# Optimization experiments

Measured on AMD Instinct MI355X. Metric: run time of the kernel, lower is better.

## Reference

```python
import jax, jax.numpy as jnp
import numpy as np

B, T, D, H = 4, 2048, 1024, 16
DK, DV, CHUNK = D // H, 2 * D // H, 64  # head_k_dim=64, head_v_dim=128 (expand_v=2.0)
EPS = 1e-5


def setup_inputs() -> dict:
    key = jax.random.key(0)
    ks = jax.random.split(key, 6)
    s = 0.02
    return {
        "x": jax.random.normal(ks[0], (B, T, D), jnp.float32),
        "Wq": jax.random.normal(ks[1], (D, H * DK), jnp.float32) * s,
        "Wk": jax.random.normal(ks[2], (D, H * DK), jnp.float32) * s,
        "Wv": jax.random.normal(ks[3], (D, H * DV), jnp.float32) * s,
        "Wg": jax.random.normal(ks[4], (D, H * DV), jnp.float32) * s,
        "Wo": jax.random.normal(ks[5], (H * DV, D), jnp.float32) * s,
        "g_norm_w": jnp.ones((DV,), jnp.float32),
    }


def _rope(q):
    # q: [B, T, H, DK]; non-interleaved (rotate-half) rotary, base 10000
    half = DK // 2
    inv_freq = 1.0 / (10000.0 ** (jnp.arange(half, dtype=jnp.float32) / half))
    freqs = jnp.arange(T, dtype=jnp.float32)[:, None] * inv_freq  # [T, half]
    cos = jnp.cos(freqs)[None, :, None, :]
    sin = jnp.sin(freqs)[None, :, None, :]
    q1, q2 = q[..., :half], q[..., half:]
    return jnp.concatenate([q1 * cos - q2 * sin, q2 * cos + q1 * sin], axis=-1)


def reference(x, Wq, Wk, Wv, Wg, Wo, g_norm_w):
    q = _rope((x @ Wq).reshape(B, T, H, DK)) * (DK ** -0.5)
    k = _rope((x @ Wk).reshape(B, T, H, DK))
    v = (x @ Wv).reshape(B, T, H, DV)

    N = T // CHUNK
    def tochunks(t):  # [B,T,H,Dh] -> [N,B,H,C,Dh]
        return t.reshape(B, N, CHUNK, H, t.shape[-1]).transpose(1, 0, 3, 2, 4)
    qc, kc, vc = tochunks(q), tochunks(k), tochunks(v)

    # per-head RetNet decay: gamma_h = 1 - 2^{-5-h}
    gamma = 1.0 - jnp.exp2(-5.0 - jnp.arange(H, dtype=jnp.float32))  # [H]
    i = jnp.arange(CHUNK, dtype=jnp.float32)
    # intra-chunk decay mask D[h,i,j] = gamma^{i-j} for j<=i else 0
    Dmask = jnp.where(i[:, None] >= i[None, :],
                      gamma[:, None, None] ** (i[:, None] - i[None, :]), 0.0)  # [H,C,C]
    cross = gamma[:, None] ** (i + 1.0)          # [H,C] query decay vs prev state
    kdec = gamma[:, None] ** (CHUNK - 1.0 - i)   # [H,C] key decay into new state
    chunk_dec = gamma ** CHUNK                   # [H]

    def step(S, qkv):
        q_, k_, v_ = qkv  # [B,H,C,DK], [B,H,C,DK], [B,H,C,DV]
        attn = jnp.einsum('bhid,bhjd->bhij', q_, k_) * Dmask
        o = jnp.einsum('bhij,bhjv->bhiv', attn, v_)
        o = o + jnp.einsum('bhid,bhdv->bhiv', q_ * cross[None, :, :, None], S)
        S = S * chunk_dec[None, :, None, None] + \
            jnp.einsum('bhjd,bhjv->bhdv', k_ * kdec[None, :, :, None], v_)
        return S, o

    S0 = jnp.zeros((B, H, DK, DV), x.dtype)
    _, o = jax.lax.scan(step, S0, (qc, kc, vc))  # [N,B,H,C,DV]
    o = o.transpose(1, 0, 3, 2, 4).reshape(B, T, H, DV)

    # fused RMSNorm + swish gate (FusedRMSNormSwishGate)
    g = (x @ Wg).reshape(B, T, H, DV)
    o = o * jax.lax.rsqrt(jnp.mean(o * o, axis=-1, keepdims=True) + EPS) * g_norm_w
    o = o * (g * jax.nn.sigmoid(g))
    return o.reshape(B, T, H * DV) @ Wo
```

## Files before the change

### kernel.cpp

```cpp
#include <hip/hip_runtime.h>
#include <hip/hip_bf16.h>
#include <math.h>

typedef unsigned short u16;
typedef unsigned int u32;
typedef __attribute__((ext_vector_type(8))) short bf16x8;
typedef __attribute__((ext_vector_type(4))) float f32x4;


__device__ __forceinline__ u16 f2bf(float f) {
  union { float f; unsigned u; } a; a.f = f;
  unsigned u = a.u;
  unsigned r = (u + 0x7fffu + ((u >> 16) & 1u)) >> 16;
  return (u16)r;
}
__device__ __forceinline__ float bf2f(u16 s) {
  union { unsigned u; float f; } a; a.u = ((unsigned)s) << 16; return a.f;
}

__global__ void k_sentinel(float* out) {
  if (threadIdx.x == 0 && blockIdx.x == 0) out[0] = 1.0e6f;
}

__device__ __forceinline__ void split8r(const float* t, bf16x8& hi, bf16x8& lo) {
#pragma unroll
  for (int m = 0; m < 8; ++m) {
    union { float f; u32 u; } c; c.f = t[m];
    union { u32 u; float f; } hf; hf.u = c.u & 0xffff0000u;
    union { float f; u32 u; } lw; lw.f = t[m] - hf.f;
    hi[m] = (short)(u16)(c.u >> 16);
    lo[m] = (short)(u16)(lw.u >> 16);
  }
}
__device__ __forceinline__ void split8p(const float* __restrict__ p, bf16x8& hi, bf16x8& lo) {
  f32x4 a = *(const f32x4*)p;
  f32x4 b = *(const f32x4*)(p + 4);
  float t[8];
  t[0]=a[0]; t[1]=a[1]; t[2]=a[2]; t[3]=a[3]; t[4]=b[0]; t[5]=b[1]; t[6]=b[2]; t[7]=b[3];
  split8r(t, hi, lo);
}

__device__ __forceinline__ void bar_lds() {
  asm volatile("s_waitcnt lgkmcnt(0)" ::: "memory");
  __builtin_amdgcn_sched_barrier(0);
  __builtin_amdgcn_s_barrier();
}

__device__ __forceinline__ void gload16(const u16* g, u16* l) {
  __builtin_amdgcn_global_load_lds(
      (const __attribute__((address_space(1))) unsigned int*)g,
      (__attribute__((address_space(3))) unsigned int*)l, 16, 0, 0);
}

__global__ __launch_bounds__(256) void k_cvt_x(const float* __restrict__ src, u16* __restrict__ dst) {
  int i = blockIdx.x * 256 + threadIdx.x;
  float4 v = ((const float4*)src)[i];
  ushort4 o;
  o.x = f2bf(v.x); o.y = f2bf(v.y); o.z = f2bf(v.z); o.w = f2bf(v.w);
  ((ushort4*)dst)[i] = o;
}

__global__ __launch_bounds__(256) void k_transpose(const float* __restrict__ src, u16* __restrict__ dst,
                                                   int K, int N) {
  __shared__ float tile[32][33];
  int n0 = blockIdx.x * 32, k0 = blockIdx.y * 32;
  int tx = threadIdx.x & 31, ty = threadIdx.x >> 5;
  for (int r = 0; r < 32; r += 8)
    tile[ty + r][tx] = src[(size_t)(k0 + ty + r) * N + n0 + tx];
  __syncthreads();
  for (int r = 0; r < 32; r += 8)
    dst[(size_t)(n0 + ty + r) * K + k0 + tx] = f2bf(tile[tx][ty + r]);
}

template <bool BF16OUT>
__global__ __launch_bounds__(256, 2) void k_gemm(const u16* __restrict__ A, const u16* __restrict__ Bt,
                                                 void* __restrict__ Cv, int N, int K) {
  __shared__ __attribute__((aligned(16))) u16 As[128 * 32];
  __shared__ __attribute__((aligned(16))) u16 Bs[128 * 32];
  int nbx = gridDim.x;
  int id = blockIdx.y * nbx + blockIdx.x;
  int cpx = (nbx * gridDim.y) >> 3;
  int sw = (id & 7) * cpx + (id >> 3);
  int bx = sw % nbx, by = sw / nbx;
  int i0 = by * 128, n0 = bx * 128;
  int tid = threadIdx.x;
  int lane = tid & 63, w = tid >> 6;
  int wr = (w >> 1) * 64, wc = (w & 1) * 64;
  int srow = lane >> 2, scol = (lane & 3) * 8;
  f32x4 acc[4][4];
#pragma unroll
  for (int m = 0; m < 4; ++m)
#pragma unroll
    for (int n = 0; n < 4; ++n) acc[m][n] = (f32x4){0.f, 0.f, 0.f, 0.f};
  int fr = lane & 15, kb = (lane >> 4) * 8;
  for (int k0 = 0; k0 < K; k0 += 32) {
    __syncthreads();
#pragma unroll
    for (int q = 0; q < 2; ++q) {
      int s = w * 2 + q;
      gload16(&A[(size_t)(i0 + s * 16 + srow) * K + k0 + scol], &As[s * 512]);
      gload16(&Bt[(size_t)(n0 + s * 16 + srow) * K + k0 + scol], &Bs[s * 512]);
    }
    asm volatile("s_waitcnt vmcnt(0)" ::: "memory");
    __syncthreads();
    bf16x8 af[4], bfr[4];
#pragma unroll
    for (int m = 0; m < 4; ++m) af[m] = *(const bf16x8*)&As[(wr + m * 16 + fr) * 32 + kb];
#pragma unroll
    for (int n = 0; n < 4; ++n) bfr[n] = *(const bf16x8*)&Bs[(wc + n * 16 + fr) * 32 + kb];
#pragma unroll
    for (int m = 0; m < 4; ++m)
#pragma unroll
      for (int n = 0; n < 4; ++n)
        acc[m][n] = __builtin_amdgcn_mfma_f32_16x16x32_bf16(af[m], bfr[n], acc[m][n], 0, 0, 0);
  }
  int rb = (lane >> 4) * 4, cb = lane & 15;
#pragma unroll
  for (int m = 0; m < 4; ++m)
#pragma unroll
    for (int n = 0; n < 4; ++n) {
      int gr = i0 + wr + m * 16 + rb;
      int gc = n0 + wc + n * 16 + cb;
#pragma unroll
      for (int r = 0; r < 4; ++r) {
        float v = acc[m][n][r];
        if (BF16OUT) ((u16*)Cv)[(size_t)(gr + r) * N + gc] = f2bf(v);
        else         ((float*)Cv)[(size_t)(gr + r) * N + gc] = v;
      }
    }
}

__global__ __launch_bounds__(256) void k_rope(float* __restrict__ qk) {
  int idx = blockIdx.x * 256 + threadIdx.x;
  int i = idx & 31;
  int row = idx >> 5;
  int t = row & 2047;
  float invf = powf(10000.f, -(float)i * (1.f / 32.f));
  float fr = (float)t * invf;
  float s = sinf(fr), c = cosf(fr);
  float* p = qk + (size_t)row * 2048;
#pragma unroll
  for (int h = 0; h < 16; ++h) {
    int c1 = h * 64 + i, c2 = c1 + 32;
    float q1 = p[c1], q2 = p[c2];
    p[c1] = (q1 * c - q2 * s) * 0.125f;
    p[c2] = (q2 * c + q1 * s) * 0.125f;
    float k1 = p[1024 + c1], k2 = p[1024 + c2];
    p[1024 + c1] = k1 * c - k2 * s;
    p[1024 + c2] = k2 * c + k1 * s;
  }
}

__global__ __launch_bounds__(512) void k_retention(const float* __restrict__ qk, const u16* __restrict__ vg,
                                                   const float* __restrict__ gnw, u16* __restrict__ og) {
  int bh = blockIdx.x & 63, rq = blockIdx.x >> 6;
  int h = bh & 15, b = bh >> 4;
  int gi0 = rq * 16;

  __shared__ __attribute__((aligned(16))) float qs[16][68];
  __shared__ __attribute__((aligned(16))) float ks[64][68];
  __shared__ __attribute__((aligned(16))) u16 vst[128][88];
  __shared__ __attribute__((aligned(16))) u16 kta_h[8][520];
  __shared__ __attribute__((aligned(16))) u16 kta_l[8][520];
  __shared__ __attribute__((aligned(16))) u16 pa_h[8][136];
  __shared__ __attribute__((aligned(16))) u16 pa_l[8][136];
  __shared__ __attribute__((aligned(16))) u16 sst_h[8][1040];
  __shared__ __attribute__((aligned(16))) u16 sst_l[8][1040];
  __shared__ float dpow[72];
  __shared__ float ssred[8][16];

  int tid = threadIdx.x;
  int w = tid >> 6, l = tid & 63;
  int fr = l & 15, fq = l >> 4;
  float gamma = 1.f - exp2f(-5.f - (float)h);
  if (tid <= 64) dpow[tid] = powf(gamma, (float)tid);
  for (int c = tid; c < 4160; c += 512) { ((u32*)sst_h)[c] = 0; ((u32*)sst_l)[c] = 0; }
  __syncthreads();
  float cdec = dpow[64];

  int e0 = w * 16;
  float gww = gnw[e0 + fr];
  int khmax = (rq < 2) ? 1 : 2;

  int qi = tid >> 4, qd4 = (tid & 15) * 4;
  int sj = tid >> 3, sdg = (tid & 7) * 8;
  int vjp = tid & 31, ve8 = (tid >> 5) * 8;

  f32x4 Sacc[4][2];
#pragma unroll
  for (int dt = 0; dt < 4; ++dt)
#pragma unroll
    for (int nt = 0; nt < 2; ++nt) Sacc[dt][nt] = (f32x4){0.f, 0.f, 0.f, 0.f};

  f32x4 pq = (f32x4){0.f, 0.f, 0.f, 0.f};
  f32x4 pk0, pk1;
  bf16x8 pva, pvb;
  {
    int rowbase = b * 2048;
    if (tid < 256) pq = *(const f32x4*)&qk[(size_t)(rowbase + gi0 + qi) * 2048 + h * 64 + qd4];
    const float* kr = &qk[(size_t)(rowbase + sj) * 2048 + 1024 + h * 64 + sdg];
    pk0 = *(const f32x4*)kr;
    pk1 = *(const f32x4*)(kr + 4);
    const u16* vr = &vg[(size_t)(rowbase + 2 * vjp) * 4096 + h * 128 + ve8];
    pva = *(const bf16x8*)vr;
    pvb = *(const bf16x8*)(vr + 4096);
  }

  for (int n = 0; n < 32; ++n) {
    int rowbase = b * 2048 + n * 64;
    if (tid < 256) *(f32x4*)&qs[qi][qd4] = pq;
    {
      *(f32x4*)&ks[sj][sdg] = pk0;
      *(f32x4*)&ks[sj][sdg + 4] = pk1;
      float kdv = dpow[63 - sj];
      float kd[8];
#pragma unroll
      for (int m = 0; m < 4; ++m) { kd[m] = pk0[m] * kdv; kd[m + 4] = pk1[m] * kdv; }
      bf16x8 kh8, kl8;
      split8r(kd, kh8, kl8);
      int J = sj >> 3, s = sj & 7, dh = tid & 7;
#pragma unroll
      for (int m = 0; m < 8; ++m) {
        int blk = (dh * 8) | (m ^ dh);
        kta_h[J][blk * 8 + s] = (u16)kh8[m];
        kta_l[J][blk * 8 + s] = (u16)kl8[m];
      }
#pragma unroll
      for (int m = 0; m < 8; ++m)
        *(u32*)&vst[ve8 + m][2 * vjp] = (u32)(u16)pva[m] | ((u32)(u16)pvb[m] << 16);
    }
    __syncthreads();
    if (n < 31) {
      int rb2 = rowbase + 64;
      if (tid < 256) pq = *(const f32x4*)&qk[(size_t)(rb2 + gi0 + qi) * 2048 + h * 64 + qd4];
      const float* kr = &qk[(size_t)(rb2 + sj) * 2048 + 1024 + h * 64 + sdg];
      pk0 = *(const f32x4*)kr;
      pk1 = *(const f32x4*)(kr + 4);
      const u16* vr = &vg[(size_t)(rb2 + 2 * vjp) * 4096 + h * 128 + ve8];
      pva = *(const bf16x8*)vr;
      pvb = *(const bf16x8*)(vr + 4096);
    }
    if (w < 4) {
      int ct = w;
      f32x4 at = (f32x4){0.f, 0.f, 0.f, 0.f};
      if (16 * ct <= gi0 + 15) {
#pragma unroll
        for (int kh = 0; kh < 2; ++kh) {
          bf16x8 qh, ql, kbh, kbl;
          split8p(&qs[fr][kh * 32 + fq * 8], qh, ql);
          split8p(&ks[16 * ct + fr][kh * 32 + fq * 8], kbh, kbl);
          at = __builtin_amdgcn_mfma_f32_16x16x32_bf16(qh, kbh, at, 0, 0, 0);
          at = __builtin_amdgcn_mfma_f32_16x16x32_bf16(qh, kbl, at, 0, 0, 0);
          at = __builtin_amdgcn_mfma_f32_16x16x32_bf16(ql, kbh, at, 0, 0, 0);
        }
      }
      int j = 16 * ct + fr;
      int J = j >> 3, jc = j & 7;
#pragma unroll
      for (int r = 0; r < 4; ++r) {
        int i = fq * 4 + r, s = gi0 + i - j;
        float val = (s >= 0) ? at[r] * dpow[s] : 0.f;
        union { float f; u32 u; } c; c.f = val;
        union { u32 u; float f; } hf; hf.u = c.u & 0xffff0000u;
        union { float f; u32 u; } lw; lw.f = val - hf.f;
        pa_h[J][i * 8 + jc] = (u16)(c.u >> 16);
        pa_l[J][i * 8 + jc] = (u16)(lw.u >> 16);
      }
    } else if (n < 31) {
      int eb = (w - 4) * 32;
#pragma unroll
      for (int dt = 0; dt < 4; ++dt)
#pragma unroll
        for (int nt = 0; nt < 2; ++nt)
#pragma unroll
          for (int r = 0; r < 4; ++r) Sacc[dt][nt][r] *= cdec;
      bf16x8 bv[2][2];
#pragma unroll
      for (int kh2 = 0; kh2 < 2; ++kh2)
#pragma unroll
        for (int nt = 0; nt < 2; ++nt)
          bv[kh2][nt] = *(const bf16x8*)&vst[eb + nt * 16 + fr][kh2 * 32 + fq * 8];
#pragma unroll
      for (int kh2 = 0; kh2 < 2; ++kh2) {
#pragma unroll
        for (int dt = 0; dt < 4; ++dt) {
          int d = dt * 16 + fr;
          int blk = d ^ ((dt * 2 + (fr >> 3)) & 7);
          bf16x8 ah = *(const bf16x8*)&kta_h[kh2 * 4 + fq][blk * 8];
          bf16x8 al = *(const bf16x8*)&kta_l[kh2 * 4 + fq][blk * 8];
#pragma unroll
          for (int nt = 0; nt < 2; ++nt) {
            Sacc[dt][nt] = __builtin_amdgcn_mfma_f32_16x16x32_bf16(ah, bv[kh2][nt], Sacc[dt][nt], 0, 0, 0);
            Sacc[dt][nt] = __builtin_amdgcn_mfma_f32_16x16x32_bf16(al, bv[kh2][nt], Sacc[dt][nt], 0, 0, 0);
          }
        }
      }
    }
    bar_lds();
    f32x4 o1 = (f32x4){0.f, 0.f, 0.f, 0.f};
    f32x4 o2 = (f32x4){0.f, 0.f, 0.f, 0.f};
#pragma unroll
    for (int kh2 = 0; kh2 < 2; ++kh2) {
      bf16x8 qh, ql;
      split8p(&qs[fr][kh2 * 32 + fq * 8], qh, ql);
      bf16x8 sh = *(const bf16x8*)&sst_h[kh2 * 4 + fq][(e0 + fr) * 8];
      bf16x8 sl = *(const bf16x8*)&sst_l[kh2 * 4 + fq][(e0 + fr) * 8];
      o2 = __builtin_amdgcn_mfma_f32_16x16x32_bf16(qh, sh, o2, 0, 0, 0);
      o2 = __builtin_amdgcn_mfma_f32_16x16x32_bf16(qh, sl, o2, 0, 0, 0);
      o2 = __builtin_amdgcn_mfma_f32_16x16x32_bf16(ql, sh, o2, 0, 0, 0);
      if (kh2 < khmax) {
        bf16x8 ph = *(const bf16x8*)&pa_h[kh2 * 4 + fq][fr * 8];
        bf16x8 pl = *(const bf16x8*)&pa_l[kh2 * 4 + fq][fr * 8];
        bf16x8 bvv = *(const bf16x8*)&vst[e0 + fr][kh2 * 32 + fq * 8];
        o1 = __builtin_amdgcn_mfma_f32_16x16x32_bf16(ph, bvv, o1, 0, 0, 0);
        o1 = __builtin_amdgcn_mfma_f32_16x16x32_bf16(pl, bvv, o1, 0, 0, 0);
      }
    }
    float ofin[4], ssp[4];
#pragma unroll
    for (int r = 0; r < 4; ++r) {
      int gi = gi0 + fq * 4 + r;
      ofin[r] = o1[r] + dpow[gi + 1] * o2[r];
      ssp[r] = ofin[r] * ofin[r];
    }
#pragma unroll
    for (int r = 0; r < 4; ++r) {
      ssp[r] += __shfl_xor(ssp[r], 1, 64);
      ssp[r] += __shfl_xor(ssp[r], 2, 64);
      ssp[r] += __shfl_xor(ssp[r], 4, 64);
      ssp[r] += __shfl_xor(ssp[r], 8, 64);
    }
    if (fr == 0) {
#pragma unroll
      for (int r = 0; r < 4; ++r) ssred[w][fq * 4 + r] = ssp[r];
    }
    bar_lds();
#pragma unroll
    for (int r = 0; r < 4; ++r) {
      int i16 = fq * 4 + r;
      float tot = 0.f;
#pragma unroll
      for (int w2 = 0; w2 < 8; ++w2) tot += ssred[w2][i16];
      float rms = rsqrtf(tot * (1.f / 128.f) + 1e-5f);
      int grow = rowbase + gi0 + i16;
      float g = bf2f(vg[(size_t)grow * 4096 + 2048 + h * 128 + e0 + fr]);
      float y = ofin[r] * rms * gww * (g / (1.f + expf(-g)));
      og[(size_t)grow * 2048 + h * 128 + e0 + fr] = f2bf(y);
    }
    if (w >= 4 && n < 31) {
      int eb = (w - 4) * 32;
#pragma unroll
      for (int dt = 0; dt < 4; ++dt) {
        int g = dt * 2 + (fq >> 1);
#pragma unroll
        for (int nt = 0; nt < 2; ++nt) {
          int e = eb + nt * 16 + fr;
          ushort4 wh, wl;
#pragma unroll
          for (int r = 0; r < 4; ++r) {
            union { float f; u32 u; } c; c.f = Sacc[dt][nt][r];
            union { u32 u; float f; } hf; hf.u = c.u & 0xffff0000u;
            union { float f; u32 u; } lw; lw.f = Sacc[dt][nt][r] - hf.f;
            ((u16*)&wh)[r] = (u16)(c.u >> 16);
            ((u16*)&wl)[r] = (u16)(lw.u >> 16);
          }
          int idx = e * 8 + (fq & 1) * 4;
          *(ushort4*)&sst_h[g][idx] = wh;
          *(ushort4*)&sst_l[g][idx] = wl;
        }
      }
    }
  }
}

extern "C" void kernel_launch(void* const* d_in, const int* in_sizes, int n_in,
                              void* d_out, int out_size, void* d_ws, size_t ws_size,
                              hipStream_t stream) {
  const float* x   = (const float*)d_in[0];
  const float* Wq  = (const float*)d_in[1];
  const float* Wk  = (const float*)d_in[2];
  const float* Wv  = (const float*)d_in[3];
  const float* Wg  = (const float*)d_in[4];
  const float* Wo  = (const float*)d_in[5];
  const float* gnw = (const float*)d_in[6];
  float* out = (float*)d_out;

  const size_t MB = 1024 * 1024;
  char* ws = (char*)d_ws;
  u16*  xb   = (u16*)(ws + 0 * MB);
  u16*  Wqkb = (u16*)(ws + 16 * MB);
  u16*  Wvgb = (u16*)(ws + 20 * MB);
  float* qk  = (float*)(ws + 32 * MB);
  u16*  vg   = (u16*)(ws + 96 * MB);
  u16*  Wob  = (u16*)(ws + 160 * MB);
  u16*  og   = (u16*)(ws + 0 * MB);
  const size_t NEED = 164 * MB;
  if (ws_size < NEED) {
    k_sentinel<<<1, 64, 0, stream>>>(out);
    return;
  }

  k_cvt_x<<<8192, 256, 0, stream>>>(x, xb);
  k_transpose<<<dim3(32, 32), 256, 0, stream>>>(Wq, Wqkb, 1024, 1024);
  k_transpose<<<dim3(32, 32), 256, 0, stream>>>(Wk, Wqkb + (size_t)1024 * 1024, 1024, 1024);
  k_transpose<<<dim3(64, 32), 256, 0, stream>>>(Wv, Wvgb, 1024, 2048);
  k_transpose<<<dim3(64, 32), 256, 0, stream>>>(Wg, Wvgb + (size_t)2048 * 1024, 1024, 2048);
  k_transpose<<<dim3(32, 64), 256, 0, stream>>>(Wo, Wob, 2048, 1024);

  k_gemm<false><<<dim3(16, 64), 256, 0, stream>>>(xb, Wqkb, qk, 2048, 1024);
  k_gemm<true ><<<dim3(32, 64), 256, 0, stream>>>(xb, Wvgb, vg, 4096, 1024);
  k_rope<<<1024, 256, 0, stream>>>(qk);
  k_retention<<<256, 512, 0, stream>>>(qk, vg, gnw, og);
  k_gemm<false><<<dim3(8, 64), 256, 0, stream>>>(og, Wob, out, 1024, 2048);
}
```

Measured before the change: 330.4 us.

## Enlarge GEMM tiles to 256x256 with a 4-stage LDS prefetch pipeline

```diff
diff --git a/kernel.cpp b/kernel.cpp
--- a/kernel.cpp
+++ b/kernel.cpp
@@ -73,54 +73,76 @@
 }
 
 template <bool BF16OUT>
-__global__ __launch_bounds__(256, 2) void k_gemm(const u16* __restrict__ A, const u16* __restrict__ Bt,
+__global__ __launch_bounds__(512, 2) void k_gemm(const u16* __restrict__ A, const u16* __restrict__ Bt,
                                                  void* __restrict__ Cv, int N, int K) {
-  __shared__ __attribute__((aligned(16))) u16 As[128 * 32];
-  __shared__ __attribute__((aligned(16))) u16 Bs[128 * 32];
+  __shared__ __attribute__((aligned(16))) u16 As[4][256 * 32];
+  __shared__ __attribute__((aligned(16))) u16 Bs[4][256 * 32];
   int nbx = gridDim.x;
   int id = blockIdx.y * nbx + blockIdx.x;
   int cpx = (nbx * gridDim.y) >> 3;
   int sw = (id & 7) * cpx + (id >> 3);
   int bx = sw % nbx, by = sw / nbx;
-  int i0 = by * 128, n0 = bx * 128;
+  int i0 = by * 256, n0 = bx * 256;
   int tid = threadIdx.x;
   int lane = tid & 63, w = tid >> 6;
-  int wr = (w >> 1) * 64, wc = (w & 1) * 64;
-  int srow = lane >> 2, scol = (lane & 3) * 8;
-  f32x4 acc[4][4];
-#pragma unroll
-  for (int m = 0; m < 4; ++m)
+  int wm = w >> 2, wn = w & 3;
+  int fr = lane & 15, kq = lane >> 4;
+  int nkt = K >> 5;
+
+  f32x4 acc[8][4];
+#pragma unroll
+  for (int m = 0; m < 8; ++m)
 #pragma unroll
     for (int n = 0; n < 4; ++n) acc[m][n] = (f32x4){0.f, 0.f, 0.f, 0.f};
-  int fr = lane & 15, kb = (lane >> 4) * 8;
-  for (int k0 = 0; k0 < K; k0 += 32) {
-    __syncthreads();
-#pragma unroll
-    for (int q = 0; q < 2; ++q) {
-      int s = w * 2 + q;
-      gload16(&A[(size_t)(i0 + s * 16 + srow) * K + k0 + scol], &As[s * 512]);
-      gload16(&Bt[(size_t)(n0 + s * 16 + srow) * K + k0 + scol], &Bs[s * 512]);
-    }
-    asm volatile("s_waitcnt vmcnt(0)" ::: "memory");
-    __syncthreads();
-    bf16x8 af[4], bfr[4];
-#pragma unroll
-    for (int m = 0; m < 4; ++m) af[m] = *(const bf16x8*)&As[(wr + m * 16 + fr) * 32 + kb];
-#pragma unroll
-    for (int n = 0; n < 4; ++n) bfr[n] = *(const bf16x8*)&Bs[(wc + n * 16 + fr) * 32 + kb];
-#pragma unroll
-    for (int m = 0; m < 4; ++m)
+
+#define STAGE(t)                                                                    \
+  {                                                                                 \
+    int slot_ = (t) & 3;                                                            \
+    _Pragma("unroll")                                                               \
+    for (int q = 0; q < 2; ++q) {                                                   \
+      int idx = (w * 2 + q) * 64 + lane;                                            \
+      int row = idx >> 2, grp = idx & 3;                                            \
+      gload16(&A[(size_t)(i0 + row) * K + (t) * 32 + grp * 8], &As[slot_][(w * 2 + q) * 512]); \
+      gload16(&Bt[(size_t)(n0 + row) * K + (t) * 32 + grp * 8], &Bs[slot_][(w * 2 + q) * 512]); \
+    }                                                                               \
+  }
+
+  STAGE(0);
+  if (nkt > 1) STAGE(1);
+  if (nkt > 2) STAGE(2);
+
+  for (int t = 0; t < nkt; ++t) {
+    int rem = nkt - 1 - t;
+    if (rem >= 2)      asm volatile("s_waitcnt vmcnt(8)" ::: "memory");
+    else if (rem == 1) asm volatile("s_waitcnt vmcnt(4)" ::: "memory");
+    else               asm volatile("s_waitcnt vmcnt(0)" ::: "memory");
+    __builtin_amdgcn_s_barrier();
+    if (t + 3 < nkt) STAGE(t + 3);
+    int slot = t & 3;
+    bf16x8 af[8], bfr[4];
+#pragma unroll
+    for (int m = 0; m < 8; ++m)
+      af[m] = *(const bf16x8*)&As[slot][(wm * 128 + m * 16 + fr) * 32 + kq * 8];
+#pragma unroll
+    for (int n = 0; n < 4; ++n)
+      bfr[n] = *(const bf16x8*)&Bs[slot][(wn * 64 + n * 16 + fr) * 32 + kq * 8];
+    __builtin_amdgcn_s_setprio(1);
+#pragma unroll
+    for (int m = 0; m < 8; ++m)
 #pragma unroll
       for (int n = 0; n < 4; ++n)
         acc[m][n] = __builtin_amdgcn_mfma_f32_16x16x32_bf16(af[m], bfr[n], acc[m][n], 0, 0, 0);
-  }
+    __builtin_amdgcn_s_setprio(0);
+  }
+#undef STAGE
+
   int rb = (lane >> 4) * 4, cb = lane & 15;
 #pragma unroll
-  for (int m = 0; m < 4; ++m)
+  for (int m = 0; m < 8; ++m)
 #pragma unroll
     for (int n = 0; n < 4; ++n) {
-      int gr = i0 + wr + m * 16 + rb;
-      int gc = n0 + wc + n * 16 + cb;
+      int gr = i0 + wm * 128 + m * 16 + rb;
+      int gc = n0 + wn * 64 + n * 16 + cb;
 #pragma unroll
       for (int r = 0; r < 4; ++r) {
         float v = acc[m][n][r];
@@ -407,9 +429,9 @@
   k_transpose<<<dim3(64, 32), 256, 0, stream>>>(Wg, Wvgb + (size_t)2048 * 1024, 1024, 2048);
   k_transpose<<<dim3(32, 64), 256, 0, stream>>>(Wo, Wob, 2048, 1024);
 
-  k_gemm<false><<<dim3(16, 64), 256, 0, stream>>>(xb, Wqkb, qk, 2048, 1024);
-  k_gemm<true ><<<dim3(32, 64), 256, 0, stream>>>(xb, Wvgb, vg, 4096, 1024);
+  k_gemm<false><<<dim3(8, 32), 512, 0, stream>>>(xb, Wqkb, qk, 2048, 1024);
+  k_gemm<true ><<<dim3(16, 32), 512, 0, stream>>>(xb, Wvgb, vg, 4096, 1024);
   k_rope<<<1024, 256, 0, stream>>>(qk);
   k_retention<<<256, 512, 0, stream>>>(qk, vg, gnw, og);
-  k_gemm<false><<<dim3(8, 64), 256, 0, stream>>>(og, Wob, out, 1024, 2048);
-}
+  k_gemm<false><<<dim3(4, 32), 512, 0, stream>>>(og, Wob, out, 1024, 2048);
+}
```

Result: slower. 380.3 us (+15.1%).

## Fuse RoPE into the QKVG GEMM epilogue and merge the projection GEMMs

Applied to the files above, without the earlier changes.

```diff
diff --git a/kernel.cpp b/kernel.cpp
--- a/kernel.cpp
+++ b/kernel.cpp
@@ -58,6 +58,15 @@
   ushort4 o;
   o.x = f2bf(v.x); o.y = f2bf(v.y); o.z = f2bf(v.z); o.w = f2bf(v.w);
   ((ushort4*)dst)[i] = o;
+}
+
+__global__ __launch_bounds__(256) void k_ropetab(float2* __restrict__ tab) {
+  int idx = blockIdx.x * 256 + threadIdx.x;
+  int t = idx >> 5, i = idx & 31;
+  float invf = powf(10000.f, -(float)i * (1.f / 32.f));
+  float ang = (float)t * invf;
+  float2 cs; cs.x = cosf(ang); cs.y = sinf(ang);
+  tab[idx] = cs;
 }
 
 __global__ __launch_bounds__(256) void k_transpose(const float* __restrict__ src, u16* __restrict__ dst,
@@ -72,9 +81,9 @@
     dst[(size_t)(n0 + ty + r) * K + k0 + tx] = f2bf(tile[tx][ty + r]);
 }
 
-template <bool BF16OUT>
-__global__ __launch_bounds__(256, 2) void k_gemm(const u16* __restrict__ A, const u16* __restrict__ Bt,
-                                                 void* __restrict__ Cv, int N, int K) {
+__global__ __launch_bounds__(256, 2) void k_gemm_qkvg(const u16* __restrict__ A, const u16* __restrict__ Bt,
+                                                      float* __restrict__ qk, u16* __restrict__ vg,
+                                                      const float2* __restrict__ tab, int K) {
   __shared__ __attribute__((aligned(16))) u16 As[128 * 32];
   __shared__ __attribute__((aligned(16))) u16 Bs[128 * 32];
   int nbx = gridDim.x;
@@ -115,6 +124,80 @@
         acc[m][n] = __builtin_amdgcn_mfma_f32_16x16x32_bf16(af[m], bfr[n], acc[m][n], 0, 0, 0);
   }
   int rb = (lane >> 4) * 4, cb = lane & 15;
+  if (n0 < 2048) {
+    float scale = (n0 < 1024) ? 0.125f : 1.0f;
+#pragma unroll
+    for (int m = 0; m < 4; ++m)
+#pragma unroll
+      for (int n = 0; n < 2; ++n) {
+        int gc = n0 + wc + n * 16 + cb;
+        int ii = n * 16 + cb;
+#pragma unroll
+        for (int r = 0; r < 4; ++r) {
+          int gr = i0 + wr + m * 16 + rb + r;
+          int t = gr & 2047;
+          float2 cs = tab[t * 32 + ii];
+          float q1 = acc[m][n][r], q2 = acc[m][n + 2][r];
+          qk[(size_t)gr * 2048 + gc]      = (q1 * cs.x - q2 * cs.y) * scale;
+          qk[(size_t)gr * 2048 + gc + 32] = (q2 * cs.x + q1 * cs.y) * scale;
+        }
+      }
+  } else {
+#pragma unroll
+    for (int m = 0; m < 4; ++m)
+#pragma unroll
+      for (int n = 0; n < 4; ++n) {
+        int gr = i0 + wr + m * 16 + rb;
+        int gc = n0 - 2048 + wc + n * 16 + cb;
+#pragma unroll
+        for (int r = 0; r < 4; ++r)
+          vg[(size_t)(gr + r) * 4096 + gc] = f2bf(acc[m][n][r]);
+      }
+  }
+}
+
+__global__ __launch_bounds__(256, 2) void k_gemm_out(const u16* __restrict__ A, const u16* __restrict__ Bt,
+                                                     float* __restrict__ Cv, int N, int K) {
+  __shared__ __attribute__((aligned(16))) u16 As[128 * 32];
+  __shared__ __attribute__((aligned(16))) u16 Bs[128 * 32];
+  int nbx = gridDim.x;
+  int id = blockIdx.y * nbx + blockIdx.x;
+  int cpx = (nbx * gridDim.y) >> 3;
+  int sw = (id & 7) * cpx + (id >> 3);
+  int bx = sw % nbx, by = sw / nbx;
+  int i0 = by * 128, n0 = bx * 128;
+  int tid = threadIdx.x;
+  int lane = tid & 63, w = tid >> 6;
+  int wr = (w >> 1) * 64, wc = (w & 1) * 64;
+  int srow = lane >> 2, scol = (lane & 3) * 8;
+  f32x4 acc[4][4];
+#pragma unroll
+  for (int m = 0; m < 4; ++m)
+#pragma unroll
+    for (int n = 0; n < 4; ++n) acc[m][n] = (f32x4){0.f, 0.f, 0.f, 0.f};
+  int fr = lane & 15, kb = (lane >> 4) * 8;
+  for (int k0 = 0; k0 < K; k0 += 32) {
+    __syncthreads();
+#pragma unroll
+    for (int q = 0; q < 2; ++q) {
+      int s = w * 2 + q;
+      gload16(&A[(size_t)(i0 + s * 16 + srow) * K + k0 + scol], &As[s * 512]);
+      gload16(&Bt[(size_t)(n0 + s * 16 + srow) * K + k0 + scol], &Bs[s * 512]);
+    }
+    asm volatile("s_waitcnt vmcnt(0)" ::: "memory");
+    __syncthreads();
+    bf16x8 af[4], bfr[4];
+#pragma unroll
+    for (int m = 0; m < 4; ++m) af[m] = *(const bf16x8*)&As[(wr + m * 16 + fr) * 32 + kb];
+#pragma unroll
+    for (int n = 0; n < 4; ++n) bfr[n] = *(const bf16x8*)&Bs[(wc + n * 16 + fr) * 32 + kb];
+#pragma unroll
+    for (int m = 0; m < 4; ++m)
+#pragma unroll
+      for (int n = 0; n < 4; ++n)
+        acc[m][n] = __builtin_amdgcn_mfma_f32_16x16x32_bf16(af[m], bfr[n], acc[m][n], 0, 0, 0);
+  }
+  int rb = (lane >> 4) * 4, cb = lane & 15;
 #pragma unroll
   for (int m = 0; m < 4; ++m)
 #pragma unroll
@@ -122,33 +205,9 @@
       int gr = i0 + wr + m * 16 + rb;
       int gc = n0 + wc + n * 16 + cb;
 #pragma unroll
-      for (int r = 0; r < 4; ++r) {
-        float v = acc[m][n][r];
-        if (BF16OUT) ((u16*)Cv)[(size_t)(gr + r) * N + gc] = f2bf(v);
-        else         ((float*)Cv)[(size_t)(gr + r) * N + gc] = v;
-      }
-    }
-}
-
-__global__ __launch_bounds__(256) void k_rope(float* __restrict__ qk) {
-  int idx = blockIdx.x * 256 + threadIdx.x;
-  int i = idx & 31;
-  int row = idx >> 5;
-  int t = row & 2047;
-  float invf = powf(10000.f, -(float)i * (1.f / 32.f));
-  float fr = (float)t * invf;
-  float s = sinf(fr), c = cosf(fr);
-  float* p = qk + (size_t)row * 2048;
-#pragma unroll
-  for (int h = 0; h < 16; ++h) {
-    int c1 = h * 64 + i, c2 = c1 + 32;
-    float q1 = p[c1], q2 = p[c2];
-    p[c1] = (q1 * c - q2 * s) * 0.125f;
-    p[c2] = (q2 * c + q1 * s) * 0.125f;
-    float k1 = p[1024 + c1], k2 = p[1024 + c2];
-    p[1024 + c1] = k1 * c - k2 * s;
-    p[1024 + c2] = k2 * c + k1 * s;
-  }
+      for (int r = 0; r < 4; ++r)
+        Cv[(size_t)(gr + r) * N + gc] = acc[m][n][r];
+    }
 }
 
 __global__ __launch_bounds__(512) void k_retention(const float* __restrict__ qk, const u16* __restrict__ vg,
@@ -387,13 +446,14 @@
 
   const size_t MB = 1024 * 1024;
   char* ws = (char*)d_ws;
-  u16*  xb   = (u16*)(ws + 0 * MB);
-  u16*  Wqkb = (u16*)(ws + 16 * MB);
-  u16*  Wvgb = (u16*)(ws + 20 * MB);
-  float* qk  = (float*)(ws + 32 * MB);
-  u16*  vg   = (u16*)(ws + 96 * MB);
-  u16*  Wob  = (u16*)(ws + 160 * MB);
-  u16*  og   = (u16*)(ws + 0 * MB);
+  u16*   xb   = (u16*)(ws + 0 * MB);
+  u16*   Wqkb = (u16*)(ws + 16 * MB);
+  u16*   Wvgb = (u16*)(ws + 20 * MB);
+  float2* tab = (float2*)(ws + 28 * MB);
+  float* qk   = (float*)(ws + 32 * MB);
+  u16*   vg   = (u16*)(ws + 96 * MB);
+  u16*   Wob  = (u16*)(ws + 160 * MB);
+  u16*   og   = (u16*)(ws + 0 * MB);
   const size_t NEED = 164 * MB;
   if (ws_size < NEED) {
     k_sentinel<<<1, 64, 0, stream>>>(out);
@@ -401,15 +461,14 @@
   }
 
   k_cvt_x<<<8192, 256, 0, stream>>>(x, xb);
+  k_ropetab<<<256, 256, 0, stream>>>(tab);
   k_transpose<<<dim3(32, 32), 256, 0, stream>>>(Wq, Wqkb, 1024, 1024);
   k_transpose<<<dim3(32, 32), 256, 0, stream>>>(Wk, Wqkb + (size_t)1024 * 1024, 1024, 1024);
   k_transpose<<<dim3(64, 32), 256, 0, stream>>>(Wv, Wvgb, 1024, 2048);
   k_transpose<<<dim3(64, 32), 256, 0, stream>>>(Wg, Wvgb + (size_t)2048 * 1024, 1024, 2048);
   k_transpose<<<dim3(32, 64), 256, 0, stream>>>(Wo, Wob, 2048, 1024);
 
-  k_gemm<false><<<dim3(16, 64), 256, 0, stream>>>(xb, Wqkb, qk, 2048, 1024);
-  k_gemm<true ><<<dim3(32, 64), 256, 0, stream>>>(xb, Wvgb, vg, 4096, 1024);
-  k_rope<<<1024, 256, 0, stream>>>(qk);
+  k_gemm_qkvg<<<dim3(48, 64), 256, 0, stream>>>(xb, Wqkb, qk, vg, tab, 1024);
   k_retention<<<256, 512, 0, stream>>>(qk, vg, gnw, og);
-  k_gemm<false><<<dim3(8, 64), 256, 0, stream>>>(og, Wob, out, 1024, 2048);
-}
+  k_gemm_out<<<dim3(8, 64), 256, 0, stream>>>(og, Wob, out, 1024, 2048);
+}
```

Result: faster. 317.0 us (-4.1%).
